# Optimization experiments

Measured on AMD Instinct MI355X. Metric: run time of the kernel, lower is better.

## Reference

```python
import jax, jax.numpy as jnp
import numpy as np

NEG = -1e30  # stand-in for -inf so fully-masked rows don't NaN; they are zeroed explicitly


def setup_inputs() -> dict:
    key = jax.random.key(0)
    ks = jax.random.split(key, 10)
    B, T, D, H = 64, 1024, 512, 512
    X = jax.random.normal(ks[0], (B, T, D), dtype=jnp.float32)
    Y = jax.random.normal(ks[1], (B, T, D), dtype=jnp.float32)
    dag = jax.random.randint(ks[2], (T, T), 0, 2).astype(jnp.float32)
    s = 1.0 / np.sqrt(D)
    Wk = jax.random.normal(ks[3], (D, H), dtype=jnp.float32) * s
    bk = jax.random.normal(ks[4], (H,), dtype=jnp.float32) * 0.01
    Wq = jax.random.normal(ks[5], (D, H), dtype=jnp.float32) * s
    bq = jax.random.normal(ks[6], (H,), dtype=jnp.float32) * 0.01
    Wv = jax.random.normal(ks[7], (D, H), dtype=jnp.float32) * s
    bv = jax.random.normal(ks[8], (H,), dtype=jnp.float32) * 0.01
    return {"X": X, "Y": Y, "dag": dag, "Wk": Wk, "bk": bk,
            "Wq": Wq, "bq": bq, "Wv": Wv, "bv": bv}


def reference(X, Y, dag, Wk, bk, Wq, bq, Wv, bv):
    head_size = Wk.shape[1]
    K = X @ Wk + bk          # [B,T,H]
    Q = Y @ Wq + bq          # [B,T,H]
    V = X @ Wv + bv          # [B,T,H]
    S = jnp.einsum('bth,bsh->bts', Q, K) / (head_size ** 0.5)  # [B,T,T]
    Sp = dag.T * S                              # DAG-masked scores
    masked = Sp == 0.0                          # zeros -> -inf in original
    logits = jnp.where(masked, NEG, Sp)
    A = jax.nn.softmax(logits, axis=-1)         # [B,T,T]
    # rows that were entirely masked produce NaN in the original; zero them
    dead = jnp.all(masked, axis=-1, keepdims=True)
    A = jnp.where(dead, 0.0, A)
    O = A @ V                                   # [B,T,H]
    return O
```

## Files before the change

### kernel.cpp

```cpp
#include <hip/hip_runtime.h>


typedef __attribute__((ext_vector_type(8))) short s8v;
typedef __attribute__((ext_vector_type(4))) float f4v;
typedef __attribute__((ext_vector_type(4))) unsigned short us4;

#define MFMA16(a, b, c) __builtin_amdgcn_mfma_f32_16x16x32_bf16(a, b, c, 0, 0, 0)
#define GLOAD_LDS16(gp, lp)                                                    \
  __builtin_amdgcn_global_load_lds(                                            \
      (const __attribute__((address_space(1))) unsigned*)(gp),                 \
      (__attribute__((address_space(3))) unsigned*)(lp), 16, 0, 0)

__device__ __forceinline__ unsigned short f2b(float f) {
  union { float f; unsigned u; } v; v.f = f;
  return (unsigned short)((v.u + 0x7fffu + ((v.u >> 16) & 1u)) >> 16);
}
__device__ __forceinline__ float b2f(unsigned short h) {
  union { unsigned u; float f; } v; v.u = ((unsigned)h) << 16;
  return v.f;
}

__global__ void cvt_bf16(const float* __restrict__ in,
                         unsigned short* __restrict__ out, size_t n) {
  size_t i = ((size_t)blockIdx.x * blockDim.x + threadIdx.x) * 4;
  size_t stride = (size_t)gridDim.x * blockDim.x * 4;
  for (; i < n; i += stride) {
    f4v v = *(const f4v*)(in + i);
    us4 r;
    r.x = f2b(v.x); r.y = f2b(v.y); r.z = f2b(v.z); r.w = f2b(v.w);
    *(us4*)(out + i) = r;
  }
}

__global__ void transpose_cvt(const float* __restrict__ in,
                              unsigned short* __restrict__ out, int n) {
  __shared__ float t[32][33];
  const int bx = blockIdx.x * 32, by = blockIdx.y * 32;
  const int x = threadIdx.x, y = threadIdx.y;
#pragma unroll
  for (int dy = 0; dy < 32; dy += 8)
    t[y + dy][x] = in[(size_t)(by + y + dy) * n + bx + x];
  __syncthreads();
#pragma unroll
  for (int dy = 0; dy < 32; dy += 8)
    out[(size_t)(bx + y + dy) * n + by + x] = f2b(t[x][y + dy]);
}

__global__ __launch_bounds__(256, 2)
void gemm_nt(const unsigned short* __restrict__ A,
             const unsigned short* __restrict__ Bm,
             unsigned short* __restrict__ C, const float* __restrict__ bias,
             int M, int N, int Kd, int biasMode, float scale,
             long strideA, long strideB, long strideC) {
  A += (size_t)blockIdx.z * strideA;
  Bm += (size_t)blockIdx.z * strideB;
  C += (size_t)blockIdx.z * strideC;
  const int m0 = blockIdx.y * 128, n0 = blockIdx.x * 128;
  __shared__ unsigned short Asm[2][128 * 64];
  __shared__ unsigned short Bsm[2][128 * 64];
  const int tid = threadIdx.x;
  const int lane = tid & 63, wid = tid >> 6;
  const int wm = wid >> 1, wn = wid & 1;
  const int g = lane >> 4, lr = lane & 15;
  const size_t ldb = (size_t)Kd * 2;

  f4v acc[4][4] = {};
  const char* Ab = (const char*)A;
  const char* Bb = (const char*)Bm;

#pragma unroll
  for (int i = 0; i < 4; ++i) {
    int sb = (wid * 4 + i) * 64;
    int p = (sb + lane) * 16;
    int row = p >> 7, colb = p & 127;
    int sc = colb ^ ((row & 7) << 4);
    GLOAD_LDS16(Ab + (size_t)(m0 + row) * ldb + sc, ((char*)Asm[0]) + sb * 16);
    GLOAD_LDS16(Bb + (size_t)(n0 + row) * ldb + sc, ((char*)Bsm[0]) + sb * 16);
  }
  const int nk = Kd >> 6;
  int buf = 0;
  for (int kt = 0; kt < nk; ++kt) {
    __syncthreads();
    if (kt + 1 < nk) {
      const int kb = (kt + 1) << 7;
#pragma unroll
      for (int i = 0; i < 4; ++i) {
        int sb = (wid * 4 + i) * 64;
        int p = (sb + lane) * 16;
        int row = p >> 7, colb = p & 127;
        int sc = colb ^ ((row & 7) << 4);
        GLOAD_LDS16(Ab + (size_t)(m0 + row) * ldb + kb + sc,
                    ((char*)Asm[buf ^ 1]) + sb * 16);
        GLOAD_LDS16(Bb + (size_t)(n0 + row) * ldb + kb + sc,
                    ((char*)Bsm[buf ^ 1]) + sb * 16);
      }
    }
    const char* As = (const char*)Asm[buf];
    const char* Bs = (const char*)Bsm[buf];
#pragma unroll
    for (int ks = 0; ks < 2; ++ks) {
      s8v af[4], bfr[4];
#pragma unroll
      for (int mi = 0; mi < 4; ++mi) {
        int row = wm * 64 + mi * 16 + lr;
        int cb = (ks * 32 + g * 8) * 2;
        af[mi] = *(const s8v*)(As + row * 128 + (cb ^ ((row & 7) << 4)));
      }
#pragma unroll
      for (int ni = 0; ni < 4; ++ni) {
        int row = wn * 64 + ni * 16 + lr;
        int cb = (ks * 32 + g * 8) * 2;
        bfr[ni] = *(const s8v*)(Bs + row * 128 + (cb ^ ((row & 7) << 4)));
      }
#pragma unroll
      for (int mi = 0; mi < 4; ++mi)
#pragma unroll
        for (int ni = 0; ni < 4; ++ni)
          acc[mi][ni] = MFMA16(af[mi], bfr[ni], acc[mi][ni]);
    }
    buf ^= 1;
  }
  if (biasMode == 0) {
    float bvv[4];
#pragma unroll
    for (int ni = 0; ni < 4; ++ni) bvv[ni] = bias[n0 + wn * 64 + ni * 16 + lr];
#pragma unroll
    for (int mi = 0; mi < 4; ++mi)
#pragma unroll
      for (int r = 0; r < 4; ++r) {
        int row = m0 + wm * 64 + mi * 16 + g * 4 + r;
        size_t rb = (size_t)row * N;
#pragma unroll
        for (int ni = 0; ni < 4; ++ni)
          C[rb + n0 + wn * 64 + ni * 16 + lr] =
              f2b((acc[mi][ni][r] + bvv[ni]) * scale);
      }
  } else {
#pragma unroll
    for (int mi = 0; mi < 4; ++mi)
#pragma unroll
      for (int r = 0; r < 4; ++r) {
        int row = m0 + wm * 64 + mi * 16 + g * 4 + r;
        float bvr = bias[row];
        size_t rb = (size_t)row * N;
#pragma unroll
        for (int ni = 0; ni < 4; ++ni)
          C[rb + n0 + wn * 64 + ni * 16 + lr] = f2b(acc[mi][ni][r] + bvr);
      }
  }
}

__global__ __launch_bounds__(512, 2)
void attn_kernel(const unsigned short* __restrict__ Qb,
                 const unsigned short* __restrict__ Kb,
                 const unsigned short* __restrict__ Vt,
                 const unsigned short* __restrict__ dagT,
                 float* __restrict__ Out) {
  __shared__ unsigned short Ksm[64 * 512];
  __shared__ unsigned short Psm[128 * 64];
  __shared__ float Lsm[128];
  const int b = blockIdx.y;
  const int t0 = blockIdx.x * 128;
  const int tid = threadIdx.x, lane = tid & 63, w = tid >> 6;
  const int g = lane >> 4, lr = lane & 15;
  const size_t bTH = (size_t)b * 524288;

  s8v qf[16];
  {
    const char* Qp = (const char*)Qb + (bTH + (size_t)(t0 + 16 * w + lr) * 512) * 2;
#pragma unroll
    for (int kk = 0; kk < 16; ++kk)
      qf[kk] = *(const s8v*)(Qp + (kk * 32 + g * 8) * 2);
  }
  f4v oacc[8][4] = {};
  float lpart[4] = {0.f, 0.f, 0.f, 0.f};
  const char* Kbase = (const char*)(Kb + bTH);
  const unsigned short* Vtb = Vt + bTH;

  for (int st = 0; st < 16; ++st) {
    const int s0 = st * 64;
    {
      const char* Kp = Kbase + (size_t)s0 * 1024;
#pragma unroll
      for (int i = 0; i < 8; ++i) {
        int sb = (w * 8 + i) * 64;
        int p = (sb + lane) * 16;
        int row = p >> 10, colb = p & 1023;
        int sc = colb ^ ((row & 7) << 4);
        GLOAD_LDS16(Kp + row * 1024 + sc, ((char*)Ksm) + sb * 16);
      }
    }
    __syncthreads();
    f4v sa[4] = {};
#pragma unroll
    for (int kk = 0; kk < 16; ++kk) {
#pragma unroll
      for (int j = 0; j < 4; ++j) {
        int row = j * 16 + lr;
        int cb = (kk * 32 + g * 8) * 2;
        s8v bf = *(const s8v*)(((const char*)Ksm) + row * 1024 +
                               (cb ^ ((row & 7) << 4)));
        sa[j] = MFMA16(qf[kk], bf, sa[j]);
      }
    }
#pragma unroll
    for (int j = 0; j < 4; ++j) {
      int sidx = s0 + j * 16 + lr;
#pragma unroll
      for (int r = 0; r < 4; ++r) {
        int tloc = 16 * w + 4 * g + r;
        float mval = b2f(dagT[(size_t)(t0 + tloc) * 1024 + sidx]);
        float sp = mval * sa[j][r];
        float p = (sp == 0.0f) ? 0.0f : __expf(sp);
        lpart[r] += p;
        int pc = (j * 16 + lr) * 2;
        *(unsigned short*)(((char*)Psm) + tloc * 128 +
                           (pc ^ ((tloc & 7) << 4))) = f2b(p);
      }
    }
    __syncthreads();
#pragma unroll
    for (int ks = 0; ks < 2; ++ks) {
      s8v vf[4];
#pragma unroll
      for (int ni = 0; ni < 4; ++ni)
        vf[ni] = *(const s8v*)((const char*)(Vtb +
                     (size_t)(64 * w + 16 * ni + lr) * 1024) +
                     (s0 + ks * 32 + g * 8) * 2);
#pragma unroll
      for (int mi = 0; mi < 8; ++mi) {
        int pr = mi * 16 + lr;
        int pc = (ks * 32 + g * 8) * 2;
        s8v af = *(const s8v*)(((const char*)Psm) + pr * 128 +
                               (pc ^ ((pr & 7) << 4)));
#pragma unroll
        for (int ni = 0; ni < 4; ++ni)
          oacc[mi][ni] = MFMA16(af, vf[ni], oacc[mi][ni]);
      }
    }
  }
#pragma unroll
  for (int r = 0; r < 4; ++r) {
    float v = lpart[r];
    v += __shfl_xor(v, 1);
    v += __shfl_xor(v, 2);
    v += __shfl_xor(v, 4);
    v += __shfl_xor(v, 8);
    if (lr == 0) Lsm[16 * w + 4 * g + r] = v;
  }
  __syncthreads();
  float* Ob = Out + ((size_t)b * 1024 + t0) * 512;
#pragma unroll
  for (int mi = 0; mi < 8; ++mi)
#pragma unroll
    for (int r = 0; r < 4; ++r) {
      int tloc = mi * 16 + 4 * g + r;
      float l = Lsm[tloc];
      float inv = (l > 0.0f) ? 1.0f / l : 0.0f;
      float* rowp = Ob + (size_t)tloc * 512 + 64 * w + lr;
#pragma unroll
      for (int ni = 0; ni < 4; ++ni) rowp[ni * 16] = oacc[mi][ni][r] * inv;
    }
}

extern "C" void kernel_launch(void* const* d_in, const int* in_sizes, int n_in,
                              void* d_out, int out_size, void* d_ws,
                              size_t ws_size, hipStream_t stream) {
  const float* X   = (const float*)d_in[0];
  const float* Y   = (const float*)d_in[1];
  const float* dag = (const float*)d_in[2];
  const float* Wk  = (const float*)d_in[3];
  const float* bk  = (const float*)d_in[4];
  const float* Wq  = (const float*)d_in[5];
  const float* bq  = (const float*)d_in[6];
  const float* Wv  = (const float*)d_in[7];
  const float* bv  = (const float*)d_in[8];
  float* Out = (float*)d_out;

  char* ws = (char*)d_ws;
  unsigned short* Xb   = (unsigned short*)(ws);
  unsigned short* Yb   = (unsigned short*)(ws + 67108864);
  unsigned short* Kb   = (unsigned short*)(ws + 134217728);
  unsigned short* Qb   = (unsigned short*)(ws + 201326592);
  unsigned short* Vt   = (unsigned short*)(ws + 268435456);
  unsigned short* Wkt  = (unsigned short*)(ws + 335544320);
  unsigned short* Wqt  = (unsigned short*)(ws + 336068608);
  unsigned short* Wvt  = (unsigned short*)(ws + 336592896);
  unsigned short* dagT = (unsigned short*)(ws + 337117184);

  const size_t EL = 33554432;
  cvt_bf16<<<dim3(2048), dim3(256), 0, stream>>>(X, Xb, EL);
  cvt_bf16<<<dim3(2048), dim3(256), 0, stream>>>(Y, Yb, EL);
  transpose_cvt<<<dim3(16, 16), dim3(32, 8), 0, stream>>>(Wk, Wkt, 512);
  transpose_cvt<<<dim3(16, 16), dim3(32, 8), 0, stream>>>(Wq, Wqt, 512);
  transpose_cvt<<<dim3(16, 16), dim3(32, 8), 0, stream>>>(Wv, Wvt, 512);
  transpose_cvt<<<dim3(32, 32), dim3(32, 8), 0, stream>>>(dag, dagT, 1024);

  gemm_nt<<<dim3(4, 512, 1), dim3(256), 0, stream>>>(
      Xb, Wkt, Kb, bk, 65536, 512, 512, 0, 1.0f, 0, 0, 0);
  gemm_nt<<<dim3(4, 512, 1), dim3(256), 0, stream>>>(
      Yb, Wqt, Qb, bq, 65536, 512, 512, 0, 0.04419417382415922f, 0, 0, 0);
  gemm_nt<<<dim3(8, 4, 64), dim3(256), 0, stream>>>(
      Wvt, Xb, Vt, bv, 512, 1024, 512, 1, 1.0f, 0, (long)524288, (long)524288);

  attn_kernel<<<dim3(8, 64, 1), dim3(512), 0, stream>>>(Qb, Kb, Vt, dagT, Out);
}
```

Measured before the change: 915.0 us.

## Prefetch next K tile during PV, XCD-aware block remap, MFMA priority hints

The attention kernel now issues the global-to-LDS load of the next K tile right after the P tile is written, so it overlaps the P·V MFMAs instead of stalling at the start of each step. An extra barrier is added because the row-sum buffer now shares LDS with the P buffer. Both GEMMs and the attention kernel use a flattened 1D grid remapped so that blocks sharing a batch or row panel land on the same XCD, which aims to improve L2 reuse of K/V and weights. s_setprio is raised around the MFMA bursts to favour matrix issue across waves. The costs are somewhat more complex index math and a small risk from the aliased LDS.

```diff
diff --git a/kernel.cpp b/kernel.cpp
--- a/kernel.cpp
+++ b/kernel.cpp
@@ -51,11 +51,25 @@
              const unsigned short* __restrict__ Bm,
              unsigned short* __restrict__ C, const float* __restrict__ bias,
              int M, int N, int Kd, int biasMode, float scale,
-             long strideA, long strideB, long strideC) {
-  A += (size_t)blockIdx.z * strideA;
-  Bm += (size_t)blockIdx.z * strideB;
-  C += (size_t)blockIdx.z * strideC;
-  const int m0 = blockIdx.y * 128, n0 = blockIdx.x * 128;
+             long strideA, long strideB, long strideC, int smode) {
+  int m0, n0, z;
+  {
+    const int p = blockIdx.x;
+    const int c = p & 7, i = p >> 3;
+    if (smode == 0) {
+      z = 0;
+      m0 = (c * 64 + (i >> 2)) * 128;
+      n0 = (i & 3) * 128;
+    } else {
+      z = c * 8 + (i >> 5);
+      const int r = i & 31;
+      n0 = (r & 7) * 128;
+      m0 = (r >> 3) * 128;
+    }
+  }
+  A += (size_t)z * strideA;
+  Bm += (size_t)z * strideB;
+  C += (size_t)z * strideC;
   __shared__ unsigned short Asm[2][128 * 64];
   __shared__ unsigned short Bsm[2][128 * 64];
   const int tid = threadIdx.x;
@@ -112,11 +126,13 @@
         int cb = (ks * 32 + g * 8) * 2;
         bfr[ni] = *(const s8v*)(Bs + row * 128 + (cb ^ ((row & 7) << 4)));
       }
+      __builtin_amdgcn_s_setprio(1);
 #pragma unroll
       for (int mi = 0; mi < 4; ++mi)
 #pragma unroll
         for (int ni = 0; ni < 4; ++ni)
           acc[mi][ni] = MFMA16(af[mi], bfr[ni], acc[mi][ni]);
+      __builtin_amdgcn_s_setprio(0);
     }
     buf ^= 1;
   }
@@ -156,11 +172,15 @@
                  const unsigned short* __restrict__ Vt,
                  const unsigned short* __restrict__ dagT,
                  float* __restrict__ Out) {
-  __shared__ unsigned short Ksm[64 * 512];
-  __shared__ unsigned short Psm[128 * 64];
-  __shared__ float Lsm[128];
-  const int b = blockIdx.y;
-  const int t0 = blockIdx.x * 128;
+  __shared__ __align__(16) char smem[81920];
+  unsigned short* Ksm = (unsigned short*)smem;
+  unsigned short* Psm = (unsigned short*)(smem + 65536);
+  float* Lsm = (float*)(smem + 65536);
+
+  const int p = blockIdx.x;
+  const int b = (p & 7) + 8 * (p >> 6);
+  const int q = (p >> 3) & 7;
+  const int t0 = q * 128;
   const int tid = threadIdx.x, lane = tid & 63, w = tid >> 6;
   const int g = lane >> 4, lr = lane & 15;
   const size_t bTH = (size_t)b * 524288;
@@ -177,21 +197,24 @@
   const char* Kbase = (const char*)(Kb + bTH);
   const unsigned short* Vtb = Vt + bTH;
 
+#define STAGE_K(ST)                                                            \
+  {                                                                            \
+    const char* Kp = Kbase + (size_t)(ST) * 65536;                             \
+    _Pragma("unroll") for (int i = 0; i < 8; ++i) {                            \
+      int sb = (w * 8 + i) * 64;                                               \
+      int pp = (sb + lane) * 16;                                               \
+      int row = pp >> 10, colb = pp & 1023;                                    \
+      int sc = colb ^ ((row & 7) << 4);                                        \
+      GLOAD_LDS16(Kp + row * 1024 + sc, ((char*)Ksm) + sb * 16);               \
+    }                                                                          \
+  }
+
+  STAGE_K(0);
   for (int st = 0; st < 16; ++st) {
     const int s0 = st * 64;
-    {
-      const char* Kp = Kbase + (size_t)s0 * 1024;
-#pragma unroll
-      for (int i = 0; i < 8; ++i) {
-        int sb = (w * 8 + i) * 64;
-        int p = (sb + lane) * 16;
-        int row = p >> 10, colb = p & 1023;
-        int sc = colb ^ ((row & 7) << 4);
-        GLOAD_LDS16(Kp + row * 1024 + sc, ((char*)Ksm) + sb * 16);
-      }
-    }
     __syncthreads();
     f4v sa[4] = {};
+    __builtin_amdgcn_s_setprio(1);
 #pragma unroll
     for (int kk = 0; kk < 16; ++kk) {
 #pragma unroll
@@ -203,6 +226,7 @@
         sa[j] = MFMA16(qf[kk], bf, sa[j]);
       }
     }
+    __builtin_amdgcn_s_setprio(0);
 #pragma unroll
     for (int j = 0; j < 4; ++j) {
       int sidx = s0 + j * 16 + lr;
@@ -211,14 +235,15 @@
         int tloc = 16 * w + 4 * g + r;
         float mval = b2f(dagT[(size_t)(t0 + tloc) * 1024 + sidx]);
         float sp = mval * sa[j][r];
-        float p = (sp == 0.0f) ? 0.0f : __expf(sp);
-        lpart[r] += p;
+        float pe = (sp == 0.0f) ? 0.0f : __expf(sp);
+        lpart[r] += pe;
         int pc = (j * 16 + lr) * 2;
         *(unsigned short*)(((char*)Psm) + tloc * 128 +
-                           (pc ^ ((tloc & 7) << 4))) = f2b(p);
+                           (pc ^ ((tloc & 7) << 4))) = f2b(pe);
       }
     }
     __syncthreads();
+    if (st + 1 < 16) STAGE_K(st + 1);
 #pragma unroll
     for (int ks = 0; ks < 2; ++ks) {
       s8v vf[4];
@@ -233,12 +258,15 @@
         int pc = (ks * 32 + g * 8) * 2;
         s8v af = *(const s8v*)(((const char*)Psm) + pr * 128 +
                                (pc ^ ((pr & 7) << 4)));
+        __builtin_amdgcn_s_setprio(1);
 #pragma unroll
         for (int ni = 0; ni < 4; ++ni)
           oacc[mi][ni] = MFMA16(af, vf[ni], oacc[mi][ni]);
-      }
-    }
-  }
+        __builtin_amdgcn_s_setprio(0);
+      }
+    }
+  }
+  __syncthreads();
 #pragma unroll
   for (int r = 0; r < 4; ++r) {
     float v = lpart[r];
@@ -261,6 +289,7 @@
 #pragma unroll
       for (int ni = 0; ni < 4; ++ni) rowp[ni * 16] = oacc[mi][ni][r] * inv;
     }
+#undef STAGE_K
 }
 
 extern "C" void kernel_launch(void* const* d_in, const int* in_sizes, int n_in,
@@ -296,12 +325,12 @@
   transpose_cvt<<<dim3(16, 16), dim3(32, 8), 0, stream>>>(Wv, Wvt, 512);
   transpose_cvt<<<dim3(32, 32), dim3(32, 8), 0, stream>>>(dag, dagT, 1024);
 
-  gemm_nt<<<dim3(4, 512, 1), dim3(256), 0, stream>>>(
-      Xb, Wkt, Kb, bk, 65536, 512, 512, 0, 1.0f, 0, 0, 0);
-  gemm_nt<<<dim3(4, 512, 1), dim3(256), 0, stream>>>(
-      Yb, Wqt, Qb, bq, 65536, 512, 512, 0, 0.04419417382415922f, 0, 0, 0);
-  gemm_nt<<<dim3(8, 4, 64), dim3(256), 0, stream>>>(
-      Wvt, Xb, Vt, bv, 512, 1024, 512, 1, 1.0f, 0, (long)524288, (long)524288);
-
-  attn_kernel<<<dim3(8, 64, 1), dim3(512), 0, stream>>>(Qb, Kb, Vt, dagT, Out);
-}
+  gemm_nt<<<dim3(2048), dim3(256), 0, stream>>>(
+      Xb, Wkt, Kb, bk, 65536, 512, 512, 0, 1.0f, 0, 0, 0, 0);
+  gemm_nt<<<dim3(2048), dim3(256), 0, stream>>>(
+      Yb, Wqt, Qb, bq, 65536, 512, 512, 0, 0.04419417382415922f, 0, 0, 0, 0);
+  gemm_nt<<<dim3(2048), dim3(256), 0, stream>>>(
+      Wvt, Xb, Vt, bv, 512, 1024, 512, 1, 1.0f, 0, (long)524288, (long)524288, 1);
+
+  attn_kernel<<<dim3(512), dim3(512), 0, stream>>>(Qb, Kb, Vt, dagT, Out);
+}
```

Measured after the change: 944.1 us. 1.03x slower.
